# Optimization experiments

Measured on AMD Instinct MI355X. Metric: run time of the kernel, lower is better.

## Reference

```python
import jax, jax.numpy as jnp
import numpy as np

B, S, DIM, H = 2, 4096, 512, 8
HD = DIM // H
SCALE = HD ** -0.5
EPS = 1e-5


def setup_inputs() -> dict:
    key = jax.random.key(0)
    ks = jax.random.split(key, 7)
    std = DIM ** -0.5
    return {
        "x": jax.random.normal(ks[0], (B, S, DIM), dtype=jnp.float32),
        "ln_gamma": jnp.ones((DIM,), jnp.float32),
        "ln_beta": jnp.zeros((DIM,), jnp.float32),
        "w_q": jax.random.normal(ks[1], (DIM, DIM), jnp.float32) * std,
        "w_k": jax.random.normal(ks[2], (DIM, DIM), jnp.float32) * std,
        "w_v": jax.random.normal(ks[3], (DIM, DIM), jnp.float32) * std,
        "w_fc": jax.random.normal(ks[4], (DIM, DIM), jnp.float32) * std,
    }


def reference(x, ln_gamma, ln_beta, w_q, w_k, w_v, w_fc):
    # LayerNorm over last dim
    mu = jnp.mean(x, axis=-1, keepdims=True)
    var = jnp.var(x, axis=-1, keepdims=True)
    xn = (x - mu) * jax.lax.rsqrt(var + EPS) * ln_gamma + ln_beta
    # QKV projections (torch Linear: y = x @ W.T), split into heads -> [B,H,S,HD]
    q = jnp.einsum('bsd,ed->bse', xn, w_q).reshape(B, S, H, HD).transpose(0, 2, 1, 3)
    k = jnp.einsum('bsd,ed->bse', xn, w_k).reshape(B, S, H, HD).transpose(0, 2, 1, 3)
    v = jnp.einsum('bsd,ed->bse', xn, w_v).reshape(B, S, H, HD).transpose(0, 2, 1, 3)
    # scores [B,H,S,S]
    attn = jnp.einsum('bhqd,bhkd->bhqk', q, k) * SCALE
    attn = jax.nn.softmax(attn, axis=-1)
    # dropout is identity in eval mode
    out = jnp.einsum('bhqk,bhkd->bhqd', attn, v)
    out = out.transpose(0, 2, 1, 3).reshape(B, S, DIM)
    return jnp.einsum('bsd,ed->bse', out, w_fc)
```

## Files before the change

### kernel.cpp

```cpp
#include <hip/hip_runtime.h>
#include <cstdint>
#include <cstddef>

typedef unsigned short u16;
typedef unsigned int   u32;
typedef __bf16 bf16x8 __attribute__((ext_vector_type(8)));
typedef float  f32x4  __attribute__((ext_vector_type(4)));
typedef float  f32x16 __attribute__((ext_vector_type(16)));
typedef u16    u16x8  __attribute__((ext_vector_type(8)));
typedef u16    u16x4  __attribute__((ext_vector_type(4)));
typedef u32    u32x2  __attribute__((ext_vector_type(2)));
typedef u32    u32x4  __attribute__((ext_vector_type(4)));

#define DI __device__ __forceinline__

constexpr int SEQ = 4096;
constexpr int DIM = 512;
constexpr int NH  = 8;
constexpr int HD  = 64;
constexpr float ATT_C1 = 0.125f * 1.44269504088896340736f;

DI u16 f2bf(float f) {
  u32 u = __builtin_bit_cast(u32, f);
  u += 0x7fffu + ((u >> 16) & 1u);
  return (u16)(u >> 16);
}

DI u32 pk2(float hi, float lo) {
  u32 uh = __builtin_bit_cast(u32, hi) + 0x8000u;
  u32 ul = __builtin_bit_cast(u32, lo) + 0x8000u;
  return __builtin_amdgcn_perm(uh, ul, 0x07060302u);
}

DI u32 cvtpk(float a, float b) {
  u32 r;
  asm("v_cvt_pk_bf16_f32 %0, %1, %2" : "=v"(r) : "v"(a), "v"(b));
  return r;
}

DI void plswap(u32& a, u32& b) {
  asm("v_permlane32_swap_b32 %0, %1" : "+v"(a), "+v"(b));
}

__global__ __launch_bounds__(256) void wconv_kernel(
    const float* __restrict__ wq, const float* __restrict__ wk,
    const float* __restrict__ wv, const float* __restrict__ wfc,
    u16* __restrict__ Wb)
{
  const int idx  = blockIdx.x * 256 + threadIdx.x;
  const int base = idx * 8;
  const int mat  = base >> 18;
  const int off  = base & (512 * 512 - 1);
  const float* src = (mat == 0) ? wq : (mat == 1) ? wk : (mat == 2) ? wv : wfc;
  const float4 a = *(const float4*)(src + off);
  const float4 b = *(const float4*)(src + off + 4);
  u32x4 o = { pk2(a.y, a.x), pk2(a.w, a.z), pk2(b.y, b.x), pk2(b.w, b.z) };
  *(u32x4*)(Wb + base) = o;
}

__global__ __launch_bounds__(256) void ln_cast_kernel(
    const float* __restrict__ x, const float* __restrict__ gamma,
    const float* __restrict__ beta, u16* __restrict__ xn)
{
  const int row  = blockIdx.x * 4 + (threadIdx.x >> 6);
  const int lane = threadIdx.x & 63;
  const float* xr = x + (size_t)row * DIM + lane * 8;
  const float4 a = *(const float4*)xr;
  const float4 b = *(const float4*)(xr + 4);
  float s = a.x + a.y + a.z + a.w + b.x + b.y + b.z + b.w;
  float q = a.x*a.x + a.y*a.y + a.z*a.z + a.w*a.w
          + b.x*b.x + b.y*b.y + b.z*b.z + b.w*b.w;
#pragma unroll
  for (int m = 1; m < 64; m <<= 1) {
    s += __shfl_xor(s, m, 64);
    q += __shfl_xor(q, m, 64);
  }
  const float mu = s * (1.0f / DIM);
  const float rs = rsqrtf(q * (1.0f / DIM) - mu * mu + 1e-5f);
  const float4 g0 = *(const float4*)(gamma + lane * 8);
  const float4 g1 = *(const float4*)(gamma + lane * 8 + 4);
  const float4 e0 = *(const float4*)(beta + lane * 8);
  const float4 e1 = *(const float4*)(beta + lane * 8 + 4);
  const float v0 = (a.x - mu) * rs * g0.x + e0.x;
  const float v1 = (a.y - mu) * rs * g0.y + e0.y;
  const float v2 = (a.z - mu) * rs * g0.z + e0.z;
  const float v3 = (a.w - mu) * rs * g0.w + e0.w;
  const float v4 = (b.x - mu) * rs * g1.x + e1.x;
  const float v5 = (b.y - mu) * rs * g1.y + e1.y;
  const float v6 = (b.z - mu) * rs * g1.z + e1.z;
  const float v7 = (b.w - mu) * rs * g1.w + e1.w;
  u32x4 o = { pk2(v1, v0), pk2(v3, v2), pk2(v5, v4), pk2(v7, v6) };
  *(u32x4*)(xn + (size_t)row * DIM + lane * 8) = o;
}

template<int MODE>
__global__ __launch_bounds__(256, 2) void gemm_kernel(
    const u16* __restrict__ A, const u16* __restrict__ Wb,
    u16* __restrict__ Qo, u16* __restrict__ Ko, u16* __restrict__ Vt,
    float* __restrict__ Co)
{
  __shared__ u16 As[128][72];
  __shared__ u16 Bs[128][72];
  const int m0 = blockIdx.y * 128, n0 = blockIdx.x * 128;
  const int t = threadIdx.x, wave = t >> 6, lane = t & 63;
  const int quad = lane >> 4, l15 = lane & 15;
  const int wm = wave >> 1, wn = wave & 1;
  const u16* Wsrc;
  if (MODE == 0) {
    const int mat = n0 >> 9;
    Wsrc = Wb + (size_t)mat * 512 * 512 + (size_t)(n0 & 511) * DIM;
  } else {
    Wsrc = Wb + (size_t)3 * 512 * 512 + (size_t)n0 * DIM;
  }

  f32x4 acc[4][4];
#pragma unroll
  for (int i = 0; i < 4; i++)
#pragma unroll
    for (int j = 0; j < 4; j++)
#pragma unroll
      for (int r = 0; r < 4; r++) acc[i][j][r] = 0.0f;

  for (int kk = 0; kk < DIM; kk += 64) {
    __syncthreads();
#pragma unroll
    for (int it = 0; it < 4; it++) {
      const int c4 = t + it * 256;
      const int r = c4 >> 3, off = (c4 & 7) * 8;
      *(u16x8*)&As[r][off] =
          *(const u16x8*)(A + (size_t)(m0 + r) * DIM + kk + off);
      *(u16x8*)&Bs[r][off] =
          *(const u16x8*)(Wsrc + (size_t)r * DIM + kk + off);
    }
    __syncthreads();
#pragma unroll
    for (int kx = 0; kx < 2; kx++) {
      bf16x8 af[4], bfr[4];
#pragma unroll
      for (int i = 0; i < 4; i++)
        af[i] = *(const bf16x8*)&As[wm * 64 + i * 16 + l15][kx * 32 + quad * 8];
#pragma unroll
      for (int j = 0; j < 4; j++)
        bfr[j] = *(const bf16x8*)&Bs[wn * 64 + j * 16 + l15][kx * 32 + quad * 8];
#pragma unroll
      for (int i = 0; i < 4; i++)
#pragma unroll
        for (int j = 0; j < 4; j++)
          acc[i][j] = __builtin_amdgcn_mfma_f32_16x16x32_bf16(
              af[i], bfr[j], acc[i][j], 0, 0, 0);
    }
  }

  if (MODE == 1) {
#pragma unroll
    for (int i = 0; i < 4; i++) {
      const int m = m0 + wm * 64 + i * 16 + quad * 4;
#pragma unroll
      for (int j = 0; j < 4; j++) {
        const int n = n0 + wn * 64 + j * 16 + l15;
#pragma unroll
        for (int r = 0; r < 4; r++)
          Co[(size_t)(m + r) * DIM + n] = acc[i][j][r];
      }
    }
  } else {
    const int mat = n0 >> 9;
    const float qs = (mat == 0) ? ATT_C1 : 1.0f;
#pragma unroll
    for (int i = 0; i < 4; i++) {
      const int m = m0 + wm * 64 + i * 16 + quad * 4;
      const int b = m >> 12, s = m & 4095;
#pragma unroll
      for (int j = 0; j < 4; j++) {
        const int ng = (n0 & 511) + wn * 64 + j * 16 + l15;
        const int h = ng >> 6, d = ng & 63;
        if (mat < 2) {
          u16* dst = (mat == 0 ? Qo : Ko) +
                     ((size_t)(b * NH + h) * SEQ) * HD + d;
#pragma unroll
          for (int r = 0; r < 4; r++)
            dst[(size_t)(s + r) * HD] = f2bf(acc[i][j][r] * qs);
        } else {
          u32x2 w;
          w[0] = pk2(acc[i][j][1], acc[i][j][0]);
          w[1] = pk2(acc[i][j][3], acc[i][j][2]);
          *(u32x2*)&Vt[((size_t)(b * NH + h) * HD + d) * SEQ + s] = w;
        }
      }
    }
  }
}

__global__ __launch_bounds__(256, 4) void attn_kernel(
    const u16* __restrict__ Q, const u16* __restrict__ K,
    const u16* __restrict__ Vt, u16* __restrict__ O)
{
  __shared__ __align__(16) char smem[36864];
  const int flat = blockIdx.x + 64 * blockIdx.y;
  const int slot = flat >> 3;
  const int bh = (flat & 7) * 2 + (slot & 1);
  const int qt = slot >> 1;
  const int b = bh >> 3, h = bh & 7;
  const int t = threadIdx.x;
  const int wave = t >> 6, lane = t & 63;
  const int kg = wave >> 1;
  const int qsub = wave & 1;
  const int tg = t & 127;
  const int l31 = lane & 31, hf = lane >> 5;

  u16 (*Kl)[72] = (u16 (*)[72])(smem + kg * 18432);
  u16 (*Vl)[72] = (u16 (*)[72])(smem + kg * 18432 + 9216);

  const u16* Qb = Q + (size_t)bh * SEQ * HD;
  const u16* Kb = K + (size_t)bh * SEQ * HD;
  const u16* Vb = Vt + (size_t)bh * HD * SEQ;
  const int qw = qt * 64 + qsub * 32;
  const int kc0 = kg * 2048;

  bf16x8 bq[4];
#pragma unroll
  for (int kk = 0; kk < 4; kk++)
    bq[kk] = *(const bf16x8*)(Qb + (size_t)(qw + l31) * HD + kk * 16 + hf * 8);

  f32x16 oacc[2];
#pragma unroll
  for (int mt = 0; mt < 2; mt++)
#pragma unroll
    for (int r = 0; r < 16; r++) oacc[mt][r] = 0.0f;
  float lrun = 0.0f;

  u16x8 kst[4], vst[4];
#pragma unroll
  for (int it = 0; it < 4; it++) {
    const int c4 = tg + it * 128;
    const int r = c4 >> 3, off = (c4 & 7) * 8;
    kst[it] = *(const u16x8*)(Kb + (size_t)(kc0 + r) * HD + off);
    vst[it] = *(const u16x8*)(Vb + (size_t)r * SEQ + kc0 + off);
  }

  for (int it2 = 0; it2 < 32; it2++) {
    const int kc = kc0 + it2 * 64;
    __syncthreads();
#pragma unroll
    for (int it = 0; it < 4; it++) {
      const int c4 = tg + it * 128;
      const int r = c4 >> 3, off = (c4 & 7) * 8;
      *(u16x8*)&Kl[r][off] = kst[it];
      *(u16x8*)&Vl[r][off] = vst[it];
    }
    __syncthreads();
    if (it2 < 31) {
#pragma unroll
      for (int it = 0; it < 4; it++) {
        const int c4 = tg + it * 128;
        const int r = c4 >> 3, off = (c4 & 7) * 8;
        kst[it] = *(const u16x8*)(Kb + (size_t)(kc + 64 + r) * HD + off);
        vst[it] = *(const u16x8*)(Vb + (size_t)r * SEQ + kc + 64 + off);
      }
    }

#pragma unroll
    for (int mt = 0; mt < 2; mt++) {
      f32x16 s;
#pragma unroll
      for (int r = 0; r < 16; r++) s[r] = 0.0f;
      __builtin_amdgcn_s_setprio(1);
#pragma unroll
      for (int kk = 0; kk < 4; kk++) {
        const bf16x8 ka =
            *(const bf16x8*)&Kl[mt * 32 + l31][kk * 16 + hf * 8];
        s = __builtin_amdgcn_mfma_f32_32x32x16_bf16(ka, bq[kk], s, 0, 0, 0);
      }
      __builtin_amdgcn_s_setprio(0);

#pragma unroll
      for (int r = 0; r < 16; r++) s[r] = __builtin_amdgcn_exp2f(s[r]);
      lrun += (((s[0] + s[1]) + (s[2] + s[3])) +
               ((s[4] + s[5]) + (s[6] + s[7]))) +
              (((s[8] + s[9]) + (s[10] + s[11])) +
               ((s[12] + s[13]) + (s[14] + s[15])));

      u32 a0 = cvtpk(s[0],  s[1]),  a1 = cvtpk(s[2],  s[3]);
      u32 a2 = cvtpk(s[4],  s[5]),  a3 = cvtpk(s[6],  s[7]);
      plswap(a0, a2); plswap(a1, a3);
      u32 c0 = cvtpk(s[8],  s[9]),  c1 = cvtpk(s[10], s[11]);
      u32 c2 = cvtpk(s[12], s[13]), c3 = cvtpk(s[14], s[15]);
      plswap(c0, c2); plswap(c1, c3);
      u32x4 f0v = { a0, a1, a2, a3 };
      u32x4 f1v = { c0, c1, c2, c3 };
      const bf16x8 p0 = __builtin_bit_cast(bf16x8, f0v);
      const bf16x8 p1 = __builtin_bit_cast(bf16x8, f1v);

      __builtin_amdgcn_s_setprio(1);
#pragma unroll
      for (int mt2 = 0; mt2 < 2; mt2++) {
        const bf16x8 va0 =
            *(const bf16x8*)&Vl[mt2 * 32 + l31][(mt * 2 + 0) * 16 + hf * 8];
        oacc[mt2] = __builtin_amdgcn_mfma_f32_32x32x16_bf16(
            va0, p0, oacc[mt2], 0, 0, 0);
        const bf16x8 va1 =
            *(const bf16x8*)&Vl[mt2 * 32 + l31][(mt * 2 + 1) * 16 + hf * 8];
        oacc[mt2] = __builtin_amdgcn_mfma_f32_32x32x16_bf16(
            va1, p1, oacc[mt2], 0, 0, 0);
      }
      __builtin_amdgcn_s_setprio(0);
    }
  }

  __syncthreads();
  f32x4 (*Rbuf)[8][64] = (f32x4 (*)[8][64])smem;
  float (*Lbuf)[64]    = (float (*)[64])(smem + 16384);
  if (kg == 1) {
#pragma unroll
    for (int mt2 = 0; mt2 < 2; mt2++)
#pragma unroll
      for (int gi = 0; gi < 4; gi++) {
        f32x4 w;
#pragma unroll
        for (int r = 0; r < 4; r++) w[r] = oacc[mt2][gi * 4 + r];
        Rbuf[qsub][mt2 * 4 + gi][lane] = w;
      }
    Lbuf[qsub][lane] = lrun;
  }
  __syncthreads();
  if (kg == 0) {
#pragma unroll
    for (int mt2 = 0; mt2 < 2; mt2++)
#pragma unroll
      for (int gi = 0; gi < 4; gi++) {
        const f32x4 w = Rbuf[qsub][mt2 * 4 + gi][lane];
#pragma unroll
        for (int r = 0; r < 4; r++) oacc[mt2][gi * 4 + r] += w[r];
      }
    lrun += Lbuf[qsub][lane];

    const float lt = lrun + __shfl_xor(lrun, 32, 64);
    const float inv = 1.0f / lt;
    const int s = qw + l31;
    u16* Ob = O + ((size_t)(b * SEQ + s)) * DIM + h * HD;
#pragma unroll
    for (int mt2 = 0; mt2 < 2; mt2++)
#pragma unroll
      for (int g = 0; g < 4; g++) {
        u32x2 w;
        w[0] = pk2(oacc[mt2][g * 4 + 1] * inv, oacc[mt2][g * 4 + 0] * inv);
        w[1] = pk2(oacc[mt2][g * 4 + 3] * inv, oacc[mt2][g * 4 + 2] * inv);
        *(u32x2*)&Ob[mt2 * 32 + g * 8 + hf * 4] = w;
      }
  }
}

extern "C" void kernel_launch(void* const* d_in, const int* in_sizes, int n_in,
                              void* d_out, int out_size, void* d_ws,
                              size_t ws_size, hipStream_t stream)
{
  const float* x     = (const float*)d_in[0];
  const float* gamma = (const float*)d_in[1];
  const float* beta  = (const float*)d_in[2];
  const float* wq    = (const float*)d_in[3];
  const float* wk    = (const float*)d_in[4];
  const float* wv    = (const float*)d_in[5];
  const float* wfc   = (const float*)d_in[6];
  float* out = (float*)d_out;

  char* ws = (char*)d_ws;
  u16* xn = (u16*)(ws);
  u16* Qb = (u16*)(ws + ((size_t)8  << 20));
  u16* Kb = (u16*)(ws + ((size_t)16 << 20));
  u16* Vt = (u16*)(ws + ((size_t)24 << 20));
  u16* Ob = (u16*)(ws + ((size_t)32 << 20));
  u16* Wb = (u16*)(ws + ((size_t)40 << 20));

  wconv_kernel<<<512, 256, 0, stream>>>(wq, wk, wv, wfc, Wb);
  ln_cast_kernel<<<2048, 256, 0, stream>>>(x, gamma, beta, xn);
  gemm_kernel<0><<<dim3(12, 64), 256, 0, stream>>>(xn, Wb, Qb, Kb, Vt, nullptr);
  attn_kernel<<<dim3(64, 16), 256, 0, stream>>>(Qb, Kb, Vt, Ob);
  gemm_kernel<1><<<dim3(4, 64), 256, 0, stream>>>(
      Ob, Wb, nullptr, nullptr, nullptr, out);
}
```

Measured before the change: 206.4 us.

## Process two 32-row query tiles per wave to reuse K/V fragments

Each wave now handles 64 query rows (two 32-row halves) instead of 32, so every K and V fragment read from shared memory feeds two MFMAs. The block's query tile doubles to 128 rows and the grid halves to 512 blocks, with launch bounds relaxed to 2 blocks per CU to allow the doubled accumulator registers. This cuts LDS traffic and global K/V staging per query row, at the cost of higher register pressure, lower occupancy, and fewer blocks to spread across the CUs.

```diff
diff --git a/kernel.cpp b/kernel.cpp
--- a/kernel.cpp
+++ b/kernel.cpp
@@ -191,12 +191,12 @@
   }
 }
 
-__global__ __launch_bounds__(256, 4) void attn_kernel(
+__global__ __launch_bounds__(256, 2) void attn_kernel(
     const u16* __restrict__ Q, const u16* __restrict__ K,
     const u16* __restrict__ Vt, u16* __restrict__ O)
 {
   __shared__ __align__(16) char smem[36864];
-  const int flat = blockIdx.x + 64 * blockIdx.y;
+  const int flat = blockIdx.x + 32 * blockIdx.y;
   const int slot = flat >> 3;
   const int bh = (flat & 7) * 2 + (slot & 1);
   const int qt = slot >> 1;
@@ -214,20 +214,25 @@
   const u16* Qb = Q + (size_t)bh * SEQ * HD;
   const u16* Kb = K + (size_t)bh * SEQ * HD;
   const u16* Vb = Vt + (size_t)bh * HD * SEQ;
-  const int qw = qt * 64 + qsub * 32;
+  const int qw = qt * 128 + qsub * 64;
   const int kc0 = kg * 2048;
 
-  bf16x8 bq[4];
-#pragma unroll
-  for (int kk = 0; kk < 4; kk++)
-    bq[kk] = *(const bf16x8*)(Qb + (size_t)(qw + l31) * HD + kk * 16 + hf * 8);
-
-  f32x16 oacc[2];
-#pragma unroll
-  for (int mt = 0; mt < 2; mt++)
-#pragma unroll
-    for (int r = 0; r < 16; r++) oacc[mt][r] = 0.0f;
-  float lrun = 0.0f;
+  bf16x8 bq[2][4];
+#pragma unroll
+  for (int qh = 0; qh < 2; qh++)
+#pragma unroll
+    for (int kk = 0; kk < 4; kk++)
+      bq[qh][kk] = *(const bf16x8*)(
+          Qb + (size_t)(qw + qh * 32 + l31) * HD + kk * 16 + hf * 8);
+
+  f32x16 oacc[2][2];
+#pragma unroll
+  for (int qh = 0; qh < 2; qh++)
+#pragma unroll
+    for (int mt2 = 0; mt2 < 2; mt2++)
+#pragma unroll
+      for (int r = 0; r < 16; r++) oacc[qh][mt2][r] = 0.0f;
+  float lrun0 = 0.0f, lrun1 = 0.0f;
 
   u16x8 kst[4], vst[4];
 #pragma unroll
@@ -261,92 +266,120 @@
 
 #pragma unroll
     for (int mt = 0; mt < 2; mt++) {
-      f32x16 s;
-#pragma unroll
-      for (int r = 0; r < 16; r++) s[r] = 0.0f;
+      f32x16 s0, s1;
+#pragma unroll
+      for (int r = 0; r < 16; r++) { s0[r] = 0.0f; s1[r] = 0.0f; }
       __builtin_amdgcn_s_setprio(1);
 #pragma unroll
       for (int kk = 0; kk < 4; kk++) {
         const bf16x8 ka =
             *(const bf16x8*)&Kl[mt * 32 + l31][kk * 16 + hf * 8];
-        s = __builtin_amdgcn_mfma_f32_32x32x16_bf16(ka, bq[kk], s, 0, 0, 0);
+        s0 = __builtin_amdgcn_mfma_f32_32x32x16_bf16(ka, bq[0][kk], s0, 0, 0, 0);
+        s1 = __builtin_amdgcn_mfma_f32_32x32x16_bf16(ka, bq[1][kk], s1, 0, 0, 0);
       }
       __builtin_amdgcn_s_setprio(0);
 
 #pragma unroll
-      for (int r = 0; r < 16; r++) s[r] = __builtin_amdgcn_exp2f(s[r]);
-      lrun += (((s[0] + s[1]) + (s[2] + s[3])) +
-               ((s[4] + s[5]) + (s[6] + s[7]))) +
-              (((s[8] + s[9]) + (s[10] + s[11])) +
-               ((s[12] + s[13]) + (s[14] + s[15])));
-
-      u32 a0 = cvtpk(s[0],  s[1]),  a1 = cvtpk(s[2],  s[3]);
-      u32 a2 = cvtpk(s[4],  s[5]),  a3 = cvtpk(s[6],  s[7]);
+      for (int r = 0; r < 16; r++) s0[r] = __builtin_amdgcn_exp2f(s0[r]);
+      lrun0 += (((s0[0] + s0[1]) + (s0[2] + s0[3])) +
+                ((s0[4] + s0[5]) + (s0[6] + s0[7]))) +
+               (((s0[8] + s0[9]) + (s0[10] + s0[11])) +
+                ((s0[12] + s0[13]) + (s0[14] + s0[15])));
+#pragma unroll
+      for (int r = 0; r < 16; r++) s1[r] = __builtin_amdgcn_exp2f(s1[r]);
+      lrun1 += (((s1[0] + s1[1]) + (s1[2] + s1[3])) +
+                ((s1[4] + s1[5]) + (s1[6] + s1[7]))) +
+               (((s1[8] + s1[9]) + (s1[10] + s1[11])) +
+                ((s1[12] + s1[13]) + (s1[14] + s1[15])));
+
+      u32 a0 = cvtpk(s0[0],  s0[1]),  a1 = cvtpk(s0[2],  s0[3]);
+      u32 a2 = cvtpk(s0[4],  s0[5]),  a3 = cvtpk(s0[6],  s0[7]);
       plswap(a0, a2); plswap(a1, a3);
-      u32 c0 = cvtpk(s[8],  s[9]),  c1 = cvtpk(s[10], s[11]);
-      u32 c2 = cvtpk(s[12], s[13]), c3 = cvtpk(s[14], s[15]);
+      u32 c0 = cvtpk(s0[8],  s0[9]),  c1 = cvtpk(s0[10], s0[11]);
+      u32 c2 = cvtpk(s0[12], s0[13]), c3 = cvtpk(s0[14], s0[15]);
       plswap(c0, c2); plswap(c1, c3);
-      u32x4 f0v = { a0, a1, a2, a3 };
-      u32x4 f1v = { c0, c1, c2, c3 };
-      const bf16x8 p0 = __builtin_bit_cast(bf16x8, f0v);
-      const bf16x8 p1 = __builtin_bit_cast(bf16x8, f1v);
+      u32x4 p00v = { a0, a1, a2, a3 };
+      u32x4 p01v = { c0, c1, c2, c3 };
+      u32 d0 = cvtpk(s1[0],  s1[1]),  d1 = cvtpk(s1[2],  s1[3]);
+      u32 d2 = cvtpk(s1[4],  s1[5]),  d3 = cvtpk(s1[6],  s1[7]);
+      plswap(d0, d2); plswap(d1, d3);
+      u32 e0 = cvtpk(s1[8],  s1[9]),  e1 = cvtpk(s1[10], s1[11]);
+      u32 e2 = cvtpk(s1[12], s1[13]), e3 = cvtpk(s1[14], s1[15]);
+      plswap(e0, e2); plswap(e1, e3);
+      u32x4 p10v = { d0, d1, d2, d3 };
+      u32x4 p11v = { e0, e1, e2, e3 };
+      const bf16x8 p00 = __builtin_bit_cast(bf16x8, p00v);
+      const bf16x8 p01 = __builtin_bit_cast(bf16x8, p01v);
+      const bf16x8 p10 = __builtin_bit_cast(bf16x8, p10v);
+      const bf16x8 p11 = __builtin_bit_cast(bf16x8, p11v);
 
       __builtin_amdgcn_s_setprio(1);
 #pragma unroll
       for (int mt2 = 0; mt2 < 2; mt2++) {
         const bf16x8 va0 =
             *(const bf16x8*)&Vl[mt2 * 32 + l31][(mt * 2 + 0) * 16 + hf * 8];
-        oacc[mt2] = __builtin_amdgcn_mfma_f32_32x32x16_bf16(
-            va0, p0, oacc[mt2], 0, 0, 0);
+        oacc[0][mt2] = __builtin_amdgcn_mfma_f32_32x32x16_bf16(
+            va0, p00, oacc[0][mt2], 0, 0, 0);
+        oacc[1][mt2] = __builtin_amdgcn_mfma_f32_32x32x16_bf16(
+            va0, p10, oacc[1][mt2], 0, 0, 0);
         const bf16x8 va1 =
             *(const bf16x8*)&Vl[mt2 * 32 + l31][(mt * 2 + 1) * 16 + hf * 8];
-        oacc[mt2] = __builtin_amdgcn_mfma_f32_32x32x16_bf16(
-            va1, p1, oacc[mt2], 0, 0, 0);
+        oacc[0][mt2] = __builtin_amdgcn_mfma_f32_32x32x16_bf16(
+            va1, p01, oacc[0][mt2], 0, 0, 0);
+        oacc[1][mt2] = __builtin_amdgcn_mfma_f32_32x32x16_bf16(
+            va1, p11, oacc[1][mt2], 0, 0, 0);
       }
       __builtin_amdgcn_s_setprio(0);
     }
   }
 
   __syncthreads();
-  f32x4 (*Rbuf)[8][64] = (f32x4 (*)[8][64])smem;
-  float (*Lbuf)[64]    = (float (*)[64])(smem + 16384);
+  f32x4 (*Rbuf)[2][8][64] = (f32x4 (*)[2][8][64])smem;
+  float (*Lbuf)[2][64]    = (float (*)[2][64])(smem + 32768);
   if (kg == 1) {
 #pragma unroll
-    for (int mt2 = 0; mt2 < 2; mt2++)
-#pragma unroll
-      for (int gi = 0; gi < 4; gi++) {
-        f32x4 w;
-#pragma unroll
-        for (int r = 0; r < 4; r++) w[r] = oacc[mt2][gi * 4 + r];
-        Rbuf[qsub][mt2 * 4 + gi][lane] = w;
-      }
-    Lbuf[qsub][lane] = lrun;
+    for (int qh = 0; qh < 2; qh++) {
+#pragma unroll
+      for (int mt2 = 0; mt2 < 2; mt2++)
+#pragma unroll
+        for (int gi = 0; gi < 4; gi++) {
+          f32x4 w;
+#pragma unroll
+          for (int r = 0; r < 4; r++) w[r] = oacc[qh][mt2][gi * 4 + r];
+          Rbuf[qsub][qh][mt2 * 4 + gi][lane] = w;
+        }
+      Lbuf[qsub][qh][lane] = (qh == 0) ? lrun0 : lrun1;
+    }
   }
   __syncthreads();
   if (kg == 0) {
 #pragma unroll
-    for (int mt2 = 0; mt2 < 2; mt2++)
-#pragma unroll
-      for (int gi = 0; gi < 4; gi++) {
-        const f32x4 w = Rbuf[qsub][mt2 * 4 + gi][lane];
-#pragma unroll
-        for (int r = 0; r < 4; r++) oacc[mt2][gi * 4 + r] += w[r];
-      }
-    lrun += Lbuf[qsub][lane];
-
-    const float lt = lrun + __shfl_xor(lrun, 32, 64);
-    const float inv = 1.0f / lt;
-    const int s = qw + l31;
-    u16* Ob = O + ((size_t)(b * SEQ + s)) * DIM + h * HD;
-#pragma unroll
-    for (int mt2 = 0; mt2 < 2; mt2++)
-#pragma unroll
-      for (int g = 0; g < 4; g++) {
-        u32x2 w;
-        w[0] = pk2(oacc[mt2][g * 4 + 1] * inv, oacc[mt2][g * 4 + 0] * inv);
-        w[1] = pk2(oacc[mt2][g * 4 + 3] * inv, oacc[mt2][g * 4 + 2] * inv);
-        *(u32x2*)&Ob[mt2 * 32 + g * 8 + hf * 4] = w;
-      }
+    for (int qh = 0; qh < 2; qh++) {
+#pragma unroll
+      for (int mt2 = 0; mt2 < 2; mt2++)
+#pragma unroll
+        for (int gi = 0; gi < 4; gi++) {
+          const f32x4 w = Rbuf[qsub][qh][mt2 * 4 + gi][lane];
+#pragma unroll
+          for (int r = 0; r < 4; r++) oacc[qh][mt2][gi * 4 + r] += w[r];
+        }
+      float lr = ((qh == 0) ? lrun0 : lrun1) + Lbuf[qsub][qh][lane];
+      const float lt = lr + __shfl_xor(lr, 32, 64);
+      const float inv = 1.0f / lt;
+      const int s = qw + qh * 32 + l31;
+      u16* Ob = O + ((size_t)(b * SEQ + s)) * DIM + h * HD;
+#pragma unroll
+      for (int mt2 = 0; mt2 < 2; mt2++)
+#pragma unroll
+        for (int g = 0; g < 4; g++) {
+          u32x2 w;
+          w[0] = pk2(oacc[qh][mt2][g * 4 + 1] * inv,
+                     oacc[qh][mt2][g * 4 + 0] * inv);
+          w[1] = pk2(oacc[qh][mt2][g * 4 + 3] * inv,
+                     oacc[qh][mt2][g * 4 + 2] * inv);
+          *(u32x2*)&Ob[mt2 * 32 + g * 8 + hf * 4] = w;
+        }
+    }
   }
 }
 
@@ -374,7 +407,7 @@
   wconv_kernel<<<512, 256, 0, stream>>>(wq, wk, wv, wfc, Wb);
   ln_cast_kernel<<<2048, 256, 0, stream>>>(x, gamma, beta, xn);
   gemm_kernel<0><<<dim3(12, 64), 256, 0, stream>>>(xn, Wb, Qb, Kb, Vt, nullptr);
-  attn_kernel<<<dim3(64, 16), 256, 0, stream>>>(Qb, Kb, Vt, Ob);
+  attn_kernel<<<dim3(32, 16), 256, 0, stream>>>(Qb, Kb, Vt, Ob);
   gemm_kernel<1><<<dim3(4, 64), 256, 0, stream>>>(
       Ob, Wb, nullptr, nullptr, nullptr, out);
 }
```

New measurement: 196.7 us. -4.7%, faster.
